# Performance work log

Hardware: AMD Instinct MI355X
Metric: run time of the kernel (lower is better)

## Reference

```python
import jax, jax.numpy as jnp
import numpy as np

E = 1024
H = 16
D = E // H
EPS = 1e-5


def _layernorm(x, g, b):
    mu = jnp.mean(x, axis=-1, keepdims=True)
    var = jnp.mean(jnp.square(x - mu), axis=-1, keepdims=True)
    return (x - mu) * jax.lax.rsqrt(var + EPS) * g + b


def setup_inputs() -> dict:
    key = jax.random.key(0)
    ks = jax.random.split(key, 12)
    B, T = 2, 2048
    s_e = 1.0 / np.sqrt(E)
    s_f = 1.0 / np.sqrt(4 * E)
    return {
        "x": jax.random.normal(ks[0], (B, T, E), jnp.float32),
        "ln1_g": jnp.ones((E,), jnp.float32),
        "ln1_b": jnp.zeros((E,), jnp.float32),
        "w_qkv": jax.random.normal(ks[1], (E, 3 * E), jnp.float32) * s_e,
        "b_qkv": jnp.zeros((3 * E,), jnp.float32),
        "w_out": jax.random.normal(ks[2], (E, E), jnp.float32) * s_e,
        "b_out": jnp.zeros((E,), jnp.float32),
        "ln2_g": jnp.ones((E,), jnp.float32),
        "ln2_b": jnp.zeros((E,), jnp.float32),
        "w_fc": jax.random.normal(ks[3], (E, 4 * E), jnp.float32) * s_e,
        "b_fc": jnp.zeros((4 * E,), jnp.float32),
        "w_proj": jax.random.normal(ks[4], (4 * E, E), jnp.float32) * s_f,
        "b_proj": jnp.zeros((E,), jnp.float32),
    }


def _attn(h, w_qkv, b_qkv, w_out, b_out):
    B, T, _ = h.shape
    qkv = h @ w_qkv + b_qkv                      # [B,T,3E]
    # torch: view(B,T,H,3*D).chunk(3,-1) -> per-head interleaved q,k,v
    qkv = qkv.reshape(B, T, H, 3, D)
    q = jnp.transpose(qkv[..., 0, :], (0, 2, 1, 3))  # [B,H,T,D]
    k = jnp.transpose(qkv[..., 1, :], (0, 2, 1, 3))
    v = jnp.transpose(qkv[..., 2, :], (0, 2, 1, 3))
    scores = jnp.einsum("bhqd,bhkd->bhqk", q, k) / np.sqrt(D)
    mask = jnp.tril(jnp.ones((T, T), bool))
    scores = jnp.where(mask, scores, -jnp.inf)
    w = jax.nn.softmax(scores, axis=-1)
    out = jnp.einsum("bhqk,bhkd->bhqd", w, v)    # [B,H,T,D]
    out = jnp.transpose(out, (0, 2, 1, 3)).reshape(B, T, E)
    return out @ w_out + b_out


def reference(x, ln1_g, ln1_b, w_qkv, b_qkv, w_out, b_out,
              ln2_g, ln2_b, w_fc, b_fc, w_proj, b_proj):
    x = x + _attn(_layernorm(x, ln1_g, ln1_b), w_qkv, b_qkv, w_out, b_out)
    h = _layernorm(x, ln2_g, ln2_b)
    h = jax.nn.gelu(h @ w_fc + b_fc, approximate=True) @ w_proj + b_proj
    return x + h
```

## Files before the change

kernel.cpp:

```cpp
#include <hip/hip_runtime.h>
#include <hip/hip_bf16.h>


#define T_DIM 2048
#define E_DIM 1024
#define NH 16

using short8 = __attribute__((__ext_vector_type__(8))) short;
using f32x4  = __attribute__((__ext_vector_type__(4))) float;

static __device__ __forceinline__ f32x4 zero4() {
  f32x4 z = {0.f, 0.f, 0.f, 0.f};
  return z;
}

static __device__ __forceinline__ unsigned short f2bfbits(float f) {
  __hip_bfloat16 h = __float2bfloat16(f);
  return *reinterpret_cast<unsigned short*>(&h);
}

static __device__ __forceinline__ float gelu_tanh(float x) {
  float z = 0.7978845608028654f * (x + 0.044715f * x * x * x);
  float e = __expf(2.0f * z);
  float th = 1.0f - 2.0f / (e + 1.0f);
  return 0.5f * x * (1.0f + th);
}

__global__ __launch_bounds__(256) void prep(
    const float* __restrict__ w_qkv, const float* __restrict__ w_out,
    const float* __restrict__ w_fc, const float* __restrict__ w_proj,
    __hip_bfloat16* __restrict__ t_qkv, __hip_bfloat16* __restrict__ t_out,
    __hip_bfloat16* __restrict__ t_fc, __hip_bfloat16* __restrict__ t_proj,
    const float* __restrict__ x, const float* __restrict__ g,
    const float* __restrict__ bb, __hip_bfloat16* __restrict__ ln1o) {
  __shared__ float tl[64][65];
  const int id = blockIdx.x;
  const int t = threadIdx.x;
  if (id < 3072) {
    const float* in;
    __hip_bfloat16* out;
    int K, N, bx, by;
    if (id < 768) {
      in = w_qkv; out = t_qkv; K = 1024; N = 3072; bx = id % 48; by = id / 48;
    } else if (id < 1024) {
      const int i = id - 768;
      in = w_out; out = t_out; K = 1024; N = 1024; bx = i % 16; by = i / 16;
    } else if (id < 2048) {
      const int i = id - 1024;
      in = w_fc; out = t_fc; K = 1024; N = 4096; bx = i % 64; by = i / 64;
    } else {
      const int i = id - 2048;
      in = w_proj; out = t_proj; K = 4096; N = 1024; bx = i % 16; by = i / 16;
    }
    const int n0 = bx * 64, k0 = by * 64;
    const int rr = t >> 4;
    const int cc = (t & 15) * 4;
#pragma unroll
    for (int i = 0; i < 4; ++i) {
      const int row = rr + i * 16;
      const float4 v = *reinterpret_cast<const float4*>(&in[(size_t)(k0 + row) * N + n0 + cc]);
      tl[row][cc] = v.x; tl[row][cc + 1] = v.y; tl[row][cc + 2] = v.z; tl[row][cc + 3] = v.w;
    }
    __syncthreads();
#pragma unroll
    for (int i = 0; i < 4; ++i) {
      const int row = rr + i * 16;
      ushort4 pk;
      pk.x = f2bfbits(tl[cc + 0][row]);
      pk.y = f2bfbits(tl[cc + 1][row]);
      pk.z = f2bfbits(tl[cc + 2][row]);
      pk.w = f2bfbits(tl[cc + 3][row]);
      *reinterpret_cast<ushort4*>(&out[(size_t)(n0 + row) * K + k0 + cc]) = pk;
    }
  } else {
    const int lane = t & 63;
    const int row = (id - 3072) * 4 + (t >> 6);
    const float* xr = x + (size_t)row * E_DIM;
    float4 v[4];
    float s = 0.f, s2 = 0.f;
#pragma unroll
    for (int i = 0; i < 4; ++i) {
      v[i] = *reinterpret_cast<const float4*>(&xr[(i * 64 + lane) * 4]);
      s  += v[i].x + v[i].y + v[i].z + v[i].w;
      s2 += v[i].x * v[i].x + v[i].y * v[i].y + v[i].z * v[i].z + v[i].w * v[i].w;
    }
#pragma unroll
    for (int m = 1; m < 64; m <<= 1) { s += __shfl_xor(s, m); s2 += __shfl_xor(s2, m); }
    const float mu = s * (1.0f / E_DIM);
    const float var = s2 * (1.0f / E_DIM) - mu * mu;
    const float rstd = rsqrtf(var + 1e-5f);
    __hip_bfloat16* orow = ln1o + (size_t)row * E_DIM;
#pragma unroll
    for (int i = 0; i < 4; ++i) {
      const int col = (i * 64 + lane) * 4;
      const float4 gv = *reinterpret_cast<const float4*>(&g[col]);
      const float4 bv = *reinterpret_cast<const float4*>(&bb[col]);
      ushort4 pk;
      pk.x = f2bfbits((v[i].x - mu) * rstd * gv.x + bv.x);
      pk.y = f2bfbits((v[i].y - mu) * rstd * gv.y + bv.y);
      pk.z = f2bfbits((v[i].z - mu) * rstd * gv.z + bv.z);
      pk.w = f2bfbits((v[i].w - mu) * rstd * gv.w + bv.w);
      *reinterpret_cast<ushort4*>(&orow[col]) = pk;
    }
  }
}

__global__ __launch_bounds__(256) void layernorm_bf16(
    const float* __restrict__ x, const float* __restrict__ g, const float* __restrict__ bb,
    __hip_bfloat16* __restrict__ out) {
  const int lane = threadIdx.x & 63;
  const int row = blockIdx.x * 4 + (threadIdx.x >> 6);
  const float* xr = x + (size_t)row * E_DIM;
  float4 v[4];
  float s = 0.f, s2 = 0.f;
#pragma unroll
  for (int i = 0; i < 4; ++i) {
    v[i] = *reinterpret_cast<const float4*>(&xr[(i * 64 + lane) * 4]);
    s  += v[i].x + v[i].y + v[i].z + v[i].w;
    s2 += v[i].x * v[i].x + v[i].y * v[i].y + v[i].z * v[i].z + v[i].w * v[i].w;
  }
#pragma unroll
  for (int m = 1; m < 64; m <<= 1) { s += __shfl_xor(s, m); s2 += __shfl_xor(s2, m); }
  const float mu = s * (1.0f / E_DIM);
  const float var = s2 * (1.0f / E_DIM) - mu * mu;
  const float rstd = rsqrtf(var + 1e-5f);
  __hip_bfloat16* orow = out + (size_t)row * E_DIM;
#pragma unroll
  for (int i = 0; i < 4; ++i) {
    const int col = (i * 64 + lane) * 4;
    const float4 gv = *reinterpret_cast<const float4*>(&g[col]);
    const float4 bv = *reinterpret_cast<const float4*>(&bb[col]);
    ushort4 pk;
    pk.x = f2bfbits((v[i].x - mu) * rstd * gv.x + bv.x);
    pk.y = f2bfbits((v[i].y - mu) * rstd * gv.y + bv.y);
    pk.z = f2bfbits((v[i].z - mu) * rstd * gv.z + bv.z);
    pk.w = f2bfbits((v[i].w - mu) * rstd * gv.w + bv.w);
    *reinterpret_cast<ushort4*>(&orow[col]) = pk;
  }
}

template <int GELU_ACT, int ADD_RES, int OUT_F32, int SCALE_Q>
__global__ __launch_bounds__(256, 3) void gemm_bt(
    const __hip_bfloat16* __restrict__ A, const __hip_bfloat16* __restrict__ Bt,
    const float* __restrict__ bias, const float* __restrict__ res,
    float* __restrict__ outF, __hip_bfloat16* __restrict__ outB,
    int M, int N, int K) {
  __shared__ __hip_bfloat16 sA[2][128 * 32];
  __shared__ __hip_bfloat16 sB[2][128 * 32];
  const int tid = threadIdx.x;
  const int w = tid >> 6, l = tid & 63;
  const int lhi = l >> 4, llo = l & 15;
  const int gx = gridDim.x;
  int wg = blockIdx.y * gx + blockIdx.x;
  const int cpx = (gx * gridDim.y) >> 3;
  wg = (wg & 7) * cpx + (wg >> 3);
  const int m0 = (wg / gx) * 128, n0 = (wg % gx) * 128;
  const int wr = (w >> 1) * 64, wc = (w & 1) * 64;
  f32x4 acc[4][4];
#pragma unroll
  for (int i = 0; i < 4; ++i)
#pragma unroll
    for (int j = 0; j < 4; ++j) acc[i][j] = zero4();

  const int nt = K >> 5;
  const int cswz = (((tid & 3) ^ ((tid >> 2) & 3)) << 3);
  auto stage = [&](int buf, int t) {
    const int k0 = t << 5;
#pragma unroll
    for (int i = 0; i < 2; ++i) {
      const int r = i * 64 + (tid >> 2);
      const int e = i * 2048 + tid * 8;
      __builtin_amdgcn_global_load_lds(
          (const __attribute__((address_space(1))) void*)(A + (size_t)(m0 + r) * K + k0 + cswz),
          (__attribute__((address_space(3))) void*)(&sA[buf][e]), 16, 0, 0);
      __builtin_amdgcn_global_load_lds(
          (const __attribute__((address_space(1))) void*)(Bt + (size_t)(n0 + r) * K + k0 + cswz),
          (__attribute__((address_space(3))) void*)(&sB[buf][e]), 16, 0, 0);
    }
  };

  stage(0, 0);
  for (int t = 0; t < nt; ++t) {
    const int cur = t & 1;
    __syncthreads();
    if (t + 1 < nt) stage(cur ^ 1, t + 1);
    const __hip_bfloat16* pa = sA[cur];
    const __hip_bfloat16* pb = sB[cur];
    short8 af[4], bfr[4];
    const int gsw = (lhi ^ (llo & 3)) << 3;
#pragma unroll
    for (int i = 0; i < 4; ++i) {
      af[i]  = *reinterpret_cast<const short8*>(pa + (wr + i * 16 + llo) * 32 + gsw);
      bfr[i] = *reinterpret_cast<const short8*>(pb + (wc + i * 16 + llo) * 32 + gsw);
    }
#pragma unroll
    for (int mi = 0; mi < 4; ++mi)
#pragma unroll
      for (int ni = 0; ni < 4; ++ni)
        acc[mi][ni] = __builtin_amdgcn_mfma_f32_16x16x32_bf16(af[mi], bfr[ni], acc[mi][ni], 0, 0, 0);
  }

#pragma unroll
  for (int mi = 0; mi < 4; ++mi) {
#pragma unroll
    for (int ni = 0; ni < 4; ++ni) {
      const int row = m0 + wr + mi * 16 + lhi * 4;
      const int col = n0 + wc + ni * 16 + llo;
      const float bc = bias[col];
      float qs = 1.0f;
      if (SCALE_Q) qs = ((col % 192) < 64) ? 0.125f : 1.0f;
#pragma unroll
      for (int j = 0; j < 4; ++j) {
        float v = acc[mi][ni][j] + bc;
        if (SCALE_Q) v *= qs;
        if (GELU_ACT) v = gelu_tanh(v);
        if (ADD_RES) v += res[(size_t)(row + j) * N + col];
        if (OUT_F32) outF[(size_t)(row + j) * N + col] = v;
        else outB[(size_t)(row + j) * N + col] = __float2bfloat16(v);
      }
    }
  }
}

template <int ADD_RES, int OUT_F32>
__global__ __launch_bounds__(256, 3) void gemm_small(
    const __hip_bfloat16* __restrict__ A, const __hip_bfloat16* __restrict__ Bt,
    const float* __restrict__ bias, const float* __restrict__ res,
    float* __restrict__ outF, __hip_bfloat16* __restrict__ outB,
    int M, int N, int K) {
  __shared__ __hip_bfloat16 sA[2][64 * 32];
  __shared__ __hip_bfloat16 sB[2][128 * 32];
  const int tid = threadIdx.x;
  const int w = tid >> 6, l = tid & 63;
  const int lhi = l >> 4, llo = l & 15;
  const int gx = gridDim.x;
  int wg = blockIdx.y * gx + blockIdx.x;
  const int cpx = (gx * gridDim.y) >> 3;
  wg = (wg & 7) * cpx + (wg >> 3);
  const int m0 = (wg / gx) * 64, n0 = (wg % gx) * 128;
  const int wr = (w >> 1) * 32, wc = (w & 1) * 64;
  f32x4 acc[2][4];
#pragma unroll
  for (int i = 0; i < 2; ++i)
#pragma unroll
    for (int j = 0; j < 4; ++j) acc[i][j] = zero4();

  const int nt = K >> 5;
  const int cswz = (((tid & 3) ^ ((tid >> 2) & 3)) << 3);
  auto stage = [&](int buf, int t) {
    const int k0 = t << 5;
    {
      const int r = tid >> 2;
      const int e = tid * 8;
      __builtin_amdgcn_global_load_lds(
          (const __attribute__((address_space(1))) void*)(A + (size_t)(m0 + r) * K + k0 + cswz),
          (__attribute__((address_space(3))) void*)(&sA[buf][e]), 16, 0, 0);
    }
#pragma unroll
    for (int i = 0; i < 2; ++i) {
      const int r = i * 64 + (tid >> 2);
      const int e = i * 2048 + tid * 8;
      __builtin_amdgcn_global_load_lds(
          (const __attribute__((address_space(1))) void*)(Bt + (size_t)(n0 + r) * K + k0 + cswz),
          (__attribute__((address_space(3))) void*)(&sB[buf][e]), 16, 0, 0);
    }
  };

  stage(0, 0);
  for (int t = 0; t < nt; ++t) {
    const int cur = t & 1;
    __syncthreads();
    if (t + 1 < nt) stage(cur ^ 1, t + 1);
    const __hip_bfloat16* pa = sA[cur];
    const __hip_bfloat16* pb = sB[cur];
    short8 af[2], bfr[4];
    const int gsw = (lhi ^ (llo & 3)) << 3;
#pragma unroll
    for (int i = 0; i < 2; ++i)
      af[i] = *reinterpret_cast<const short8*>(pa + (wr + i * 16 + llo) * 32 + gsw);
#pragma unroll
    for (int i = 0; i < 4; ++i)
      bfr[i] = *reinterpret_cast<const short8*>(pb + (wc + i * 16 + llo) * 32 + gsw);
#pragma unroll
    for (int mi = 0; mi < 2; ++mi)
#pragma unroll
      for (int ni = 0; ni < 4; ++ni)
        acc[mi][ni] = __builtin_amdgcn_mfma_f32_16x16x32_bf16(af[mi], bfr[ni], acc[mi][ni], 0, 0, 0);
  }

#pragma unroll
  for (int mi = 0; mi < 2; ++mi) {
#pragma unroll
    for (int ni = 0; ni < 4; ++ni) {
      const int row = m0 + wr + mi * 16 + lhi * 4;
      const int col = n0 + wc + ni * 16 + llo;
      const float bc = bias[col];
#pragma unroll
      for (int j = 0; j < 4; ++j) {
        float v = acc[mi][ni][j] + bc;
        if (ADD_RES) v += res[(size_t)(row + j) * N + col];
        if (OUT_F32) outF[(size_t)(row + j) * N + col] = v;
        else outB[(size_t)(row + j) * N + col] = __float2bfloat16(v);
      }
    }
  }
}

__global__ __launch_bounds__(256) void transpose_v(
    const __hip_bfloat16* __restrict__ qkv, __hip_bfloat16* __restrict__ vt) {
  const int t0 = blockIdx.x * 64, h = blockIdx.y, b = blockIdx.z;
  const size_t rb = (size_t)b * T_DIM;
  const size_t obase = ((size_t)(b * NH + h) * 64) * T_DIM;
  __shared__ unsigned short tl[64][64];
  const int tid = threadIdx.x;
#pragma unroll
  for (int k = 0; k < 2; ++k) {
    const int e = k * 2048 + tid * 8;
    const int tr = e >> 6, dc = e & 63;
    const short8 v =
        *reinterpret_cast<const short8*>(qkv + (rb + t0 + tr) * 3072 + h * 192 + 128 + dc);
    *reinterpret_cast<short8*>(&tl[tr][dc ^ ((tr & 7) << 3)]) = v;
  }
  __syncthreads();
#pragma unroll
  for (int k = 0; k < 2; ++k) {
    const int e = k * 2048 + tid * 8;
    const int dr = e >> 6, tc = e & 63;
    short8 o;
#pragma unroll
    for (int jj = 0; jj < 8; ++jj)
      o[jj] = (short)tl[tc + jj][dr ^ (((tc + jj) & 7) << 3)];
    *reinterpret_cast<short8*>(&vt[obase + (size_t)dr * T_DIM + t0 + tc]) = o;
  }
}

__global__ __launch_bounds__(256) void attn_fwd(
    const __hip_bfloat16* __restrict__ qkv, const __hip_bfloat16* __restrict__ vt,
    __hip_bfloat16* __restrict__ aout) {
  const int hb = blockIdx.x;
  const int h = hb & 15, b = hb >> 4;
  const int tid = threadIdx.x, w = tid >> 6, l = tid & 63;
  const int lhi = l >> 4, llo = l & 15;
  const int pr = w >> 1;
  const int s = w & 1;
  const int p = blockIdx.y * 2 + pr;
  const size_t rb = (size_t)b * T_DIM;
  const size_t vbase = ((size_t)(b * NH + h) * 64) * T_DIM;
  __shared__ __hip_bfloat16 sP[4][32][72];
  __shared__ float mrg[2][64][49];

  short8 onesb;
#pragma unroll
  for (int i = 0; i < 8; ++i) onesb[i] = (short)0x3F80;

#pragma unroll
  for (int half = 0; half < 2; ++half) {
    const int tile = half ? (63 - p) : p;
    const int q0 = tile * 32;
    const int nkv = (tile >> 1) + 1;
    const int base = (tile & 1) << 5;
    const int kt_begin = s ? (nkv >> 1) : 0;
    const int kt_end   = s ? nkv : (nkv >> 1);

    short8 qf[2][2];
#pragma unroll
    for (int mf = 0; mf < 2; ++mf) {
      const __hip_bfloat16* qp =
          qkv + ((rb + q0 + mf * 16 + llo) * 3072 + h * 192 + lhi * 8);
      qf[mf][0] = *reinterpret_cast<const short8*>(qp);
      qf[mf][1] = *reinterpret_cast<const short8*>(qp + 32);
    }
    float mrun[2][4], lrun[2][4];
    f32x4 oacc[2][4];
#pragma unroll
    for (int mf = 0; mf < 2; ++mf)
#pragma unroll
      for (int j = 0; j < 4; ++j) { mrun[mf][j] = -1e30f; lrun[mf][j] = 0.f; }
#pragma unroll
    for (int mf = 0; mf < 2; ++mf)
#pragma unroll
      for (int di = 0; di < 4; ++di) oacc[mf][di] = zero4();

    auto loadK = [&](short8 (&dst)[4][2], int k0) {
#pragma unroll
      for (int ni = 0; ni < 4; ++ni) {
        const __hip_bfloat16* kp =
            qkv + ((rb + k0 + ni * 16 + llo) * 3072 + h * 192 + 64 + lhi * 8);
        dst[ni][0] = *reinterpret_cast<const short8*>(kp);
        dst[ni][1] = *reinterpret_cast<const short8*>(kp + 32);
      }
    };

    auto step = [&](short8 (&cK)[4][2], short8 (&nK)[4][2], int kt) {
      const bool diag = (kt == nkv - 1);
      const bool evendiag = diag && (base == 0);
      f32x4 sc[2][4];
      __builtin_amdgcn_s_setprio(1);
#pragma unroll
      for (int mf = 0; mf < 2; ++mf)
#pragma unroll
        for (int ni = 0; ni < 4; ++ni) {
          sc[mf][ni] = zero4();
          if (!evendiag || ni < 2) {
            sc[mf][ni] =
                __builtin_amdgcn_mfma_f32_16x16x32_bf16(qf[mf][0], cK[ni][0], sc[mf][ni], 0, 0, 0);
            sc[mf][ni] =
                __builtin_amdgcn_mfma_f32_16x16x32_bf16(qf[mf][1], cK[ni][1], sc[mf][ni], 0, 0, 0);
          }
        }
      __builtin_amdgcn_s_setprio(0);
      if (kt + 1 < kt_end) loadK(nK, (kt + 1) * 64);
      short8 vCur[4][2];
#pragma unroll
      for (int di = 0; di < 4; ++di) {
        const __hip_bfloat16* vp =
            vt + (vbase + (size_t)(di * 16 + llo) * T_DIM + kt * 64 + lhi * 8);
        vCur[di][0] = *reinterpret_cast<const short8*>(vp);
        vCur[di][1] = *reinterpret_cast<const short8*>(vp + 32);
      }
      float corr[2][4];
#pragma unroll
      for (int mf = 0; mf < 2; ++mf)
#pragma unroll
        for (int j = 0; j < 4; ++j) {
          const int ql = mf * 16 + lhi * 4 + j;
          float sv[4];
#pragma unroll
          for (int ni = 0; ni < 4; ++ni) {
            float sval = sc[mf][ni][j];
            if (diag) sval = (ni * 16 + llo <= base + ql) ? sval : -1e30f;
            sv[ni] = sval;
          }
          float mx = fmaxf(fmaxf(sv[0], sv[1]), fmaxf(sv[2], sv[3]));
#pragma unroll
          for (int d = 1; d < 16; d <<= 1) mx = fmaxf(mx, __shfl_xor(mx, d));
          const float mnew = fmaxf(mrun[mf][j], mx);
          const float c = __expf(mrun[mf][j] - mnew);
          mrun[mf][j] = mnew;
          corr[mf][j] = c;
#pragma unroll
          for (int ni = 0; ni < 4; ++ni)
            sP[w][mf * 16 + lhi * 4 + j][ni * 16 + llo] = __float2bfloat16(__expf(sv[ni] - mnew));
#pragma unroll
          for (int di = 0; di < 4; ++di) oacc[mf][di][j] *= c;
        }
      asm volatile("s_waitcnt lgkmcnt(0)" ::: "memory");
      __builtin_amdgcn_s_setprio(1);
#pragma unroll
      for (int mf = 0; mf < 2; ++mf) {
        const short8 pf0 = *reinterpret_cast<const short8*>(&sP[w][mf * 16 + llo][lhi * 8]);
        const short8 pf1 = *reinterpret_cast<const short8*>(&sP[w][mf * 16 + llo][32 + lhi * 8]);
        f32x4 lacc = zero4();
        lacc = __builtin_amdgcn_mfma_f32_16x16x32_bf16(pf0, onesb, lacc, 0, 0, 0);
        if (!evendiag)
          lacc = __builtin_amdgcn_mfma_f32_16x16x32_bf16(pf1, onesb, lacc, 0, 0, 0);
#pragma unroll
        for (int di = 0; di < 4; ++di) {
          oacc[mf][di] =
              __builtin_amdgcn_mfma_f32_16x16x32_bf16(pf0, vCur[di][0], oacc[mf][di], 0, 0, 0);
          if (!evendiag)
            oacc[mf][di] =
                __builtin_amdgcn_mfma_f32_16x16x32_bf16(pf1, vCur[di][1], oacc[mf][di], 0, 0, 0);
        }
#pragma unroll
        for (int j = 0; j < 4; ++j)
          lrun[mf][j] = lrun[mf][j] * corr[mf][j] + lacc[j];
      }
      __builtin_amdgcn_s_setprio(0);
    };

    short8 kA[4][2], kB[4][2];
    if (kt_begin < kt_end) loadK(kA, kt_begin * 64);
    for (int kt = kt_begin; kt < kt_end; ++kt) {
      if ((kt - kt_begin) & 1) step(kB, kA, kt);
      else                     step(kA, kB, kt);
    }

    if (s == 0) {
      float* dst = &mrg[pr][l][0];
#pragma unroll
      for (int mf = 0; mf < 2; ++mf)
#pragma unroll
        for (int di = 0; di < 4; ++di)
#pragma unroll
          for (int j = 0; j < 4; ++j) dst[(mf * 4 + di) * 4 + j] = oacc[mf][di][j];
#pragma unroll
      for (int mf = 0; mf < 2; ++mf)
#pragma unroll
        for (int j = 0; j < 4; ++j) {
          dst[32 + mf * 4 + j] = mrun[mf][j];
          dst[40 + mf * 4 + j] = lrun[mf][j];
        }
    }
    __syncthreads();
    if (s == 1) {
      const float* src = &mrg[pr][l][0];
#pragma unroll
      for (int mf = 0; mf < 2; ++mf)
#pragma unroll
        for (int j = 0; j < 4; ++j) {
          const float m0 = src[32 + mf * 4 + j], l0 = src[40 + mf * 4 + j];
          const float m1 = mrun[mf][j], l1 = lrun[mf][j];
          const float mm = fmaxf(m0, m1);
          const float a0 = __expf(m0 - mm), a1 = __expf(m1 - mm);
          const float linv = 1.0f / (l0 * a0 + l1 * a1);
          const size_t row = rb + q0 + mf * 16 + lhi * 4 + j;
#pragma unroll
          for (int di = 0; di < 4; ++di) {
            const float o = (src[(mf * 4 + di) * 4 + j] * a0 + oacc[mf][di][j] * a1) * linv;
            aout[row * 1024 + h * 64 + di * 16 + llo] = __float2bfloat16(o);
          }
        }
    }
    __syncthreads();
  }
}

extern "C" void kernel_launch(void* const* d_in, const int* in_sizes, int n_in,
                              void* d_out, int out_size, void* d_ws, size_t ws_size,
                              hipStream_t stream) {
  (void)in_sizes; (void)n_in; (void)out_size; (void)ws_size;
  const float* x      = (const float*)d_in[0];
  const float* ln1_g  = (const float*)d_in[1];
  const float* ln1_b  = (const float*)d_in[2];
  const float* w_qkv  = (const float*)d_in[3];
  const float* b_qkv  = (const float*)d_in[4];
  const float* w_out  = (const float*)d_in[5];
  const float* b_out  = (const float*)d_in[6];
  const float* ln2_g  = (const float*)d_in[7];
  const float* ln2_b  = (const float*)d_in[8];
  const float* w_fc   = (const float*)d_in[9];
  const float* b_fc   = (const float*)d_in[10];
  const float* w_proj = (const float*)d_in[11];
  const float* b_proj = (const float*)d_in[12];
  float* out = (float*)d_out;

  const int M = 2 * T_DIM;
  char* wsp = (char*)d_ws;
  size_t off = 0;
  auto carve = [&](size_t bytes) {
    void* p = wsp + off;
    off += (bytes + 255) & ~(size_t)255;
    return p;
  };
  __hip_bfloat16* wt_qkv  = (__hip_bfloat16*)carve((size_t)3072 * 1024 * 2);
  __hip_bfloat16* wt_out  = (__hip_bfloat16*)carve((size_t)1024 * 1024 * 2);
  __hip_bfloat16* wt_fc   = (__hip_bfloat16*)carve((size_t)4096 * 1024 * 2);
  __hip_bfloat16* wt_proj = (__hip_bfloat16*)carve((size_t)1024 * 4096 * 2);
  __hip_bfloat16* ln1o    = (__hip_bfloat16*)carve((size_t)M * 1024 * 2);
  __hip_bfloat16* qkvb    = (__hip_bfloat16*)carve((size_t)M * 3072 * 2);
  __hip_bfloat16* vtb     = (__hip_bfloat16*)carve((size_t)2 * NH * 64 * T_DIM * 2);
  __hip_bfloat16* attnb   = (__hip_bfloat16*)carve((size_t)M * 1024 * 2);
  float*          x2      = (float*)carve((size_t)M * 1024 * 4);
  __hip_bfloat16* h1      = (__hip_bfloat16*)carve((size_t)M * 4096 * 2);
  __hip_bfloat16* ln2o    = ln1o;

  prep<<<4096, 256, 0, stream>>>(w_qkv, w_out, w_fc, w_proj,
                                 wt_qkv, wt_out, wt_fc, wt_proj,
                                 x, ln1_g, ln1_b, ln1o);
  gemm_bt<0, 0, 0, 1><<<dim3(3072 / 128, M / 128), 256, 0, stream>>>(
      ln1o, wt_qkv, b_qkv, nullptr, nullptr, qkvb, M, 3072, 1024);
  transpose_v<<<dim3(T_DIM / 64, NH, 2), 256, 0, stream>>>(qkvb, vtb);
  attn_fwd<<<dim3(32, 16), 256, 0, stream>>>(qkvb, vtb, attnb);
  gemm_small<1, 1><<<dim3(1024 / 128, M / 64), 256, 0, stream>>>(
      attnb, wt_out, b_out, x, x2, nullptr, M, 1024, 1024);
  layernorm_bf16<<<M / 4, 256, 0, stream>>>(x2, ln2_g, ln2_b, ln2o);
  gemm_bt<1, 0, 0, 0><<<dim3(4096 / 128, M / 128), 256, 0, stream>>>(
      ln2o, wt_fc, b_fc, nullptr, nullptr, h1, M, 4096, 1024);
  gemm_small<1, 1><<<dim3(1024 / 128, M / 64), 256, 0, stream>>>(
      h1, wt_proj, b_proj, x2, out, nullptr, M, 1024, 4096);
}
```

Baseline: 296.3 us.

## Split attention KV range four ways per query tile and double the grid

Each block now handles a single query-tile pair, and its four waves split the KV range into quarters instead of two waves per tile splitting it in halves. The grid doubles and launch bounds request 4 blocks per CU, so there are more blocks to fill the machine. The per-wave K register double-buffering is dropped in favour of a simple loop, and the V load is moved between the two score halves. A four-way softmax merge through reused shared memory replaces the two-way merge, which adds barriers and merge work and may add register pressure under the tighter launch bound.

```diff
diff --git a/kernel.cpp b/kernel.cpp
--- a/kernel.cpp
+++ b/kernel.cpp
@@ -334,20 +334,19 @@
   }
 }
 
-__global__ __launch_bounds__(256) void attn_fwd(
+__global__ __launch_bounds__(256, 4) void attn_fwd(
     const __hip_bfloat16* __restrict__ qkv, const __hip_bfloat16* __restrict__ vt,
     __hip_bfloat16* __restrict__ aout) {
   const int hb = blockIdx.x;
   const int h = hb & 15, b = hb >> 4;
-  const int tid = threadIdx.x, w = tid >> 6, l = tid & 63;
+  const int tid = threadIdx.x, s4 = tid >> 6, l = tid & 63;
   const int lhi = l >> 4, llo = l & 15;
-  const int pr = w >> 1;
-  const int s = w & 1;
-  const int p = blockIdx.y * 2 + pr;
+  const int p = blockIdx.y;
   const size_t rb = (size_t)b * T_DIM;
   const size_t vbase = ((size_t)(b * NH + h) * 64) * T_DIM;
-  __shared__ __hip_bfloat16 sP[4][32][72];
-  __shared__ float mrg[2][64][49];
+  __shared__ __align__(16) unsigned char smem[4 * 32 * 72 * 2];
+  auto sP = reinterpret_cast<__hip_bfloat16(*)[32][72]>(smem);
+  float* mrgf = reinterpret_cast<float*>(smem);
 
   short8 onesb;
 #pragma unroll
@@ -359,8 +358,8 @@
     const int q0 = tile * 32;
     const int nkv = (tile >> 1) + 1;
     const int base = (tile & 1) << 5;
-    const int kt_begin = s ? (nkv >> 1) : 0;
-    const int kt_end   = s ? nkv : (nkv >> 1);
+    const int kt_begin = (s4 * nkv) >> 2;
+    const int kt_end   = ((s4 + 1) * nkv) >> 2;
 
     short8 qf[2][2];
 #pragma unroll
@@ -381,53 +380,49 @@
 #pragma unroll
       for (int di = 0; di < 4; ++di) oacc[mf][di] = zero4();
 
-    auto loadK = [&](short8 (&dst)[4][2], int k0) {
+    for (int kt = kt_begin; kt < kt_end; ++kt) {
+      const bool diag = (kt == nkv - 1);
+      const bool evendiag = diag && (base == 0);
+      const int k0 = kt * 64;
+      short8 kC[4][2];
 #pragma unroll
       for (int ni = 0; ni < 4; ++ni) {
         const __hip_bfloat16* kp =
             qkv + ((rb + k0 + ni * 16 + llo) * 3072 + h * 192 + 64 + lhi * 8);
-        dst[ni][0] = *reinterpret_cast<const short8*>(kp);
-        dst[ni][1] = *reinterpret_cast<const short8*>(kp + 32);
-      }
-    };
-
-    auto step = [&](short8 (&cK)[4][2], short8 (&nK)[4][2], int kt) {
-      const bool diag = (kt == nkv - 1);
-      const bool evendiag = diag && (base == 0);
-      f32x4 sc[2][4];
-      __builtin_amdgcn_s_setprio(1);
-#pragma unroll
-      for (int mf = 0; mf < 2; ++mf)
+        kC[ni][0] = *reinterpret_cast<const short8*>(kp);
+        kC[ni][1] = *reinterpret_cast<const short8*>(kp + 32);
+      }
+      short8 vC[4][2];
+      float corr[2][4];
+#pragma unroll
+      for (int mf = 0; mf < 2; ++mf) {
+        f32x4 sc[4];
+        __builtin_amdgcn_s_setprio(1);
 #pragma unroll
         for (int ni = 0; ni < 4; ++ni) {
-          sc[mf][ni] = zero4();
+          sc[ni] = zero4();
           if (!evendiag || ni < 2) {
-            sc[mf][ni] =
-                __builtin_amdgcn_mfma_f32_16x16x32_bf16(qf[mf][0], cK[ni][0], sc[mf][ni], 0, 0, 0);
-            sc[mf][ni] =
-                __builtin_amdgcn_mfma_f32_16x16x32_bf16(qf[mf][1], cK[ni][1], sc[mf][ni], 0, 0, 0);
+            sc[ni] = __builtin_amdgcn_mfma_f32_16x16x32_bf16(qf[mf][0], kC[ni][0], sc[ni], 0, 0, 0);
+            sc[ni] = __builtin_amdgcn_mfma_f32_16x16x32_bf16(qf[mf][1], kC[ni][1], sc[ni], 0, 0, 0);
           }
         }
-      __builtin_amdgcn_s_setprio(0);
-      if (kt + 1 < kt_end) loadK(nK, (kt + 1) * 64);
-      short8 vCur[4][2];
-#pragma unroll
-      for (int di = 0; di < 4; ++di) {
-        const __hip_bfloat16* vp =
-            vt + (vbase + (size_t)(di * 16 + llo) * T_DIM + kt * 64 + lhi * 8);
-        vCur[di][0] = *reinterpret_cast<const short8*>(vp);
-        vCur[di][1] = *reinterpret_cast<const short8*>(vp + 32);
-      }
-      float corr[2][4];
-#pragma unroll
-      for (int mf = 0; mf < 2; ++mf)
+        __builtin_amdgcn_s_setprio(0);
+        if (mf == 1) {
+#pragma unroll
+          for (int di = 0; di < 4; ++di) {
+            const __hip_bfloat16* vp =
+                vt + (vbase + (size_t)(di * 16 + llo) * T_DIM + k0 + lhi * 8);
+            vC[di][0] = *reinterpret_cast<const short8*>(vp);
+            vC[di][1] = *reinterpret_cast<const short8*>(vp + 32);
+          }
+        }
 #pragma unroll
         for (int j = 0; j < 4; ++j) {
           const int ql = mf * 16 + lhi * 4 + j;
           float sv[4];
 #pragma unroll
           for (int ni = 0; ni < 4; ++ni) {
-            float sval = sc[mf][ni][j];
+            float sval = sc[ni][j];
             if (diag) sval = (ni * 16 + llo <= base + ql) ? sval : -1e30f;
             sv[ni] = sval;
           }
@@ -440,16 +435,17 @@
           corr[mf][j] = c;
 #pragma unroll
           for (int ni = 0; ni < 4; ++ni)
-            sP[w][mf * 16 + lhi * 4 + j][ni * 16 + llo] = __float2bfloat16(__expf(sv[ni] - mnew));
+            sP[s4][mf * 16 + lhi * 4 + j][ni * 16 + llo] = __float2bfloat16(__expf(sv[ni] - mnew));
 #pragma unroll
           for (int di = 0; di < 4; ++di) oacc[mf][di][j] *= c;
         }
+      }
       asm volatile("s_waitcnt lgkmcnt(0)" ::: "memory");
       __builtin_amdgcn_s_setprio(1);
 #pragma unroll
       for (int mf = 0; mf < 2; ++mf) {
-        const short8 pf0 = *reinterpret_cast<const short8*>(&sP[w][mf * 16 + llo][lhi * 8]);
-        const short8 pf1 = *reinterpret_cast<const short8*>(&sP[w][mf * 16 + llo][32 + lhi * 8]);
+        const short8 pf0 = *reinterpret_cast<const short8*>(&sP[s4][mf * 16 + llo][lhi * 8]);
+        const short8 pf1 = *reinterpret_cast<const short8*>(&sP[s4][mf * 16 + llo][32 + lhi * 8]);
         f32x4 lacc = zero4();
         lacc = __builtin_amdgcn_mfma_f32_16x16x32_bf16(pf0, onesb, lacc, 0, 0, 0);
         if (!evendiag)
@@ -457,60 +453,59 @@
 #pragma unroll
         for (int di = 0; di < 4; ++di) {
           oacc[mf][di] =
-              __builtin_amdgcn_mfma_f32_16x16x32_bf16(pf0, vCur[di][0], oacc[mf][di], 0, 0, 0);
+              __builtin_amdgcn_mfma_f32_16x16x32_bf16(pf0, vC[di][0], oacc[mf][di], 0, 0, 0);
           if (!evendiag)
             oacc[mf][di] =
-                __builtin_amdgcn_mfma_f32_16x16x32_bf16(pf1, vCur[di][1], oacc[mf][di], 0, 0, 0);
+                __builtin_amdgcn_mfma_f32_16x16x32_bf16(pf1, vC[di][1], oacc[mf][di], 0, 0, 0);
         }
 #pragma unroll
         for (int j = 0; j < 4; ++j)
           lrun[mf][j] = lrun[mf][j] * corr[mf][j] + lacc[j];
       }
       __builtin_amdgcn_s_setprio(0);
-    };
-
-    short8 kA[4][2], kB[4][2];
-    if (kt_begin < kt_end) loadK(kA, kt_begin * 64);
-    for (int kt = kt_begin; kt < kt_end; ++kt) {
-      if ((kt - kt_begin) & 1) step(kB, kA, kt);
-      else                     step(kA, kB, kt);
-    }
-
-    if (s == 0) {
-      float* dst = &mrg[pr][l][0];
-#pragma unroll
-      for (int mf = 0; mf < 2; ++mf)
+    }
+
+#pragma unroll
+    for (int mf = 0; mf < 2; ++mf) {
+      __syncthreads();
+      if (s4 < 3) {
+        float* dst = mrgf + (s4 * 64 + l) * 24;
 #pragma unroll
         for (int di = 0; di < 4; ++di)
 #pragma unroll
-          for (int j = 0; j < 4; ++j) dst[(mf * 4 + di) * 4 + j] = oacc[mf][di][j];
-#pragma unroll
-      for (int mf = 0; mf < 2; ++mf)
+          for (int j = 0; j < 4; ++j) dst[di * 4 + j] = oacc[mf][di][j];
 #pragma unroll
         for (int j = 0; j < 4; ++j) {
-          dst[32 + mf * 4 + j] = mrun[mf][j];
-          dst[40 + mf * 4 + j] = lrun[mf][j];
+          dst[16 + j] = mrun[mf][j];
+          dst[20 + j] = lrun[mf][j];
         }
-    }
-    __syncthreads();
-    if (s == 1) {
-      const float* src = &mrg[pr][l][0];
-#pragma unroll
-      for (int mf = 0; mf < 2; ++mf)
+      }
+      __syncthreads();
+      if (s4 == 3) {
 #pragma unroll
         for (int j = 0; j < 4; ++j) {
-          const float m0 = src[32 + mf * 4 + j], l0 = src[40 + mf * 4 + j];
-          const float m1 = mrun[mf][j], l1 = lrun[mf][j];
-          const float mm = fmaxf(m0, m1);
-          const float a0 = __expf(m0 - mm), a1 = __expf(m1 - mm);
-          const float linv = 1.0f / (l0 * a0 + l1 * a1);
+          float ms[3], ls[3];
+#pragma unroll
+          for (int si = 0; si < 3; ++si) {
+            ms[si] = mrgf[(si * 64 + l) * 24 + 16 + j];
+            ls[si] = mrgf[(si * 64 + l) * 24 + 20 + j];
+          }
+          float mm = fmaxf(fmaxf(mrun[mf][j], ms[0]), fmaxf(ms[1], ms[2]));
+          float a3 = __expf(mrun[mf][j] - mm);
+          float a0 = __expf(ms[0] - mm), a1 = __expf(ms[1] - mm), a2 = __expf(ms[2] - mm);
+          const float lt = lrun[mf][j] * a3 + ls[0] * a0 + ls[1] * a1 + ls[2] * a2;
+          const float inv = 1.0f / lt;
           const size_t row = rb + q0 + mf * 16 + lhi * 4 + j;
 #pragma unroll
           for (int di = 0; di < 4; ++di) {
-            const float o = (src[(mf * 4 + di) * 4 + j] * a0 + oacc[mf][di][j] * a1) * linv;
-            aout[row * 1024 + h * 64 + di * 16 + llo] = __float2bfloat16(o);
+            const float o = oacc[mf][di][j] * a3 +
+                            mrgf[(0 * 64 + l) * 24 + di * 4 + j] * a0 +
+                            mrgf[(1 * 64 + l) * 24 + di * 4 + j] * a1 +
+                            mrgf[(2 * 64 + l) * 24 + di * 4 + j] * a2;
+            aout[row * 1024 + h * 64 + di * 16 + llo] = __float2bfloat16(o * inv);
           }
         }
+      }
     }
     __syncthreads();
   }
@@ -561,7 +556,7 @@
   gemm_bt<0, 0, 0, 1><<<dim3(3072 / 128, M / 128), 256, 0, stream>>>(
       ln1o, wt_qkv, b_qkv, nullptr, nullptr, qkvb, M, 3072, 1024);
   transpose_v<<<dim3(T_DIM / 64, NH, 2), 256, 0, stream>>>(qkvb, vtb);
-  attn_fwd<<<dim3(32, 16), 256, 0, stream>>>(qkvb, vtb, attnb);
+  attn_fwd<<<dim3(32, 32), 256, 0, stream>>>(qkvb, vtb, attnb);
   gemm_small<1, 1><<<dim3(1024 / 128, M / 64), 256, 0, stream>>>(
       attnb, wt_out, b_out, x, x2, nullptr, M, 1024, 1024);
   layernorm_bf16<<<M / 4, 256, 0, stream>>>(x2, ln2_g, ln2_b, ln2o);
```

Result: slower. 303.1 us (+2.3%).
